# Kernel optimization log

Measured on AMD Instinct MI355X. Metric: run time of the kernel, lower is better.

The kernel has to match this reference:

```python
import jax, jax.numpy as jnp
import numpy as np

N_POS, D_MODEL, D_SAE, TOP_K = 2, 1024, 32768, 32


def setup_inputs() -> dict:
    key = jax.random.key(0)
    k_x, k_we, k_wd = jax.random.split(key, 3)
    x = jax.random.normal(k_x, (4096, N_POS, D_MODEL), dtype=jnp.float32)
    W_enc = jax.random.normal(k_we, (N_POS, D_MODEL, D_SAE), dtype=jnp.float32) * (1.0 / D_MODEL ** 0.5)
    W_dec = jax.random.normal(k_wd, (D_SAE, N_POS, D_MODEL), dtype=jnp.float32) * (1.0 / D_SAE ** 0.5)
    b_enc = jnp.zeros((D_SAE,), dtype=jnp.float32)
    b_dec = jnp.zeros((N_POS, D_MODEL), dtype=jnp.float32)
    return {"x": x, "W_enc": W_enc, "W_dec": W_dec, "b_enc": b_enc, "b_dec": b_dec}


def reference(x, W_enc, W_dec, b_enc, b_dec):
    # Encode: per-position einsum then shared bias -> (batch, d_sae)
    pre_act = jnp.einsum('btd,tds->bs', x, W_enc) + b_enc
    top_vals, top_idx = jax.lax.top_k(pre_act, TOP_K)  # (b, k)
    batch = pre_act.shape[0]
    rows = jnp.arange(batch)[:, None]  # (b, 1) broadcast against (b, k)
    z = jnp.zeros_like(pre_act).at[rows, top_idx].set(jax.nn.relu(top_vals))
    # Decode: dense contraction over d_sae -> (batch, n_positions, d_model)
    x_hat = jnp.einsum('bs,std->btd', z, W_dec) + b_dec
    return x_hat
```

## Files before the change

### kernel.cpp

```cpp
#include <hip/hip_runtime.h>
#include <cstdint>
#include <cstddef>

typedef unsigned short u16;
typedef unsigned long long u64;
typedef __attribute__((ext_vector_type(8))) short short8;
typedef __attribute__((ext_vector_type(4))) float f32x4;

constexpr int K_DIM = 2048;
constexpr int S_DIM = 32768;
constexpr int TOPK  = 32;
constexpr int CAP   = 256;
#define EPS      0.06f
#define THR_EMIT 3.7f
#define HIST_LO  3.5f

__device__ __forceinline__ u16 f2bf(float f) {
    unsigned u = __float_as_uint(f);
    return (u16)((u + 0x7FFFu + ((u >> 16) & 1u)) >> 16);
}
__device__ __forceinline__ unsigned key_map(float f) {
    unsigned u = __float_as_uint(f);
    return (u & 0x80000000u) ? ~u : (u | 0x80000000u);
}
__device__ __forceinline__ float key_unmap(unsigned k) {
    unsigned u = (k & 0x80000000u) ? (k ^ 0x80000000u) : ~k;
    return __uint_as_float(u);
}

__global__ __launch_bounds__(256) void init_kernel(int* __restrict__ flag, int M)
{
    int i = blockIdx.x * 256 + threadIdx.x;
    if (i < M) flag[i] = 0;
}

__global__ __launch_bounds__(256) void conv_x_kernel(
    const float* __restrict__ x, u16* __restrict__ hi, int n4)
{
    int i = blockIdx.x * 256 + threadIdx.x;
    if (i >= n4) return;
    float4 v = ((const float4*)x)[i];
    ushort4 h;
    h.x = f2bf(v.x); h.y = f2bf(v.y); h.z = f2bf(v.z); h.w = f2bf(v.w);
    ((ushort4*)hi)[i] = h;
}

__global__ __launch_bounds__(256) void conv_wt_kernel(
    const float* __restrict__ W, float* __restrict__ WT, u16* __restrict__ Wh)
{
    __shared__ float tile[64][65];
    const int t  = threadIdx.x;
    const int s0 = blockIdx.x * 64;
    const int k0 = blockIdx.y * 64;
#pragma unroll
    for (int i = 0; i < 4; ++i) {
        int kl = (t >> 4) + i * 16;
        int sc = (t & 15) * 4;
        float4 v = *(const float4*)&W[(size_t)(k0 + kl) * S_DIM + s0 + sc];
        tile[kl][sc] = v.x; tile[kl][sc + 1] = v.y;
        tile[kl][sc + 2] = v.z; tile[kl][sc + 3] = v.w;
    }
    __syncthreads();
    const int klc = (t & 7) * 8;
#pragma unroll
    for (int i = 0; i < 2; ++i) {
        int sl = (t >> 3) + i * 32;
        float f[8];
        short8 h8;
#pragma unroll
        for (int j = 0; j < 8; ++j) {
            f[j] = tile[klc + j][sl];
            h8[j] = (short)f2bf(f[j]);
        }
        size_t o = (size_t)(s0 + sl) * K_DIM + k0 + klc;
        *(float4*)&WT[o]     = make_float4(f[0], f[1], f[2], f[3]);
        *(float4*)&WT[o + 4] = make_float4(f[4], f[5], f[6], f[7]);
        *(short8*)&Wh[o] = h8;
    }
}

__device__ __forceinline__ void gl16(const u16* g, u16* s) {
    __builtin_amdgcn_global_load_lds(
        (const __attribute__((address_space(1))) unsigned int*)g,
        (__attribute__((address_space(3))) unsigned int*)s,
        16, 0, 0);
}

#define LGKM0  do { asm volatile("s_waitcnt lgkmcnt(0)" ::: "memory"); \
                    __builtin_amdgcn_sched_barrier(0); } while (0)
#define VMW(n) asm volatile("s_waitcnt vmcnt(" #n ")" ::: "memory")
#define BAR    do { __builtin_amdgcn_s_barrier(); \
                    __builtin_amdgcn_sched_barrier(0); } while (0)

__global__ __launch_bounds__(512, 2) void gemm_mfma_kernel(
    const u16* __restrict__ A, const u16* __restrict__ B,
    const float* __restrict__ bias, float* __restrict__ C)
{
    __shared__ alignas(16) u16 sA[2][256 * 64];
    __shared__ alignas(16) u16 sB[2][256 * 64];

    const int t = threadIdx.x;
    const int lane = t & 63;
    const int w = t >> 6;
    const int wm = w >> 2, wn = w & 3;

    const int nwg = gridDim.x;
    const int q = nwg >> 3;
    const int bid = blockIdx.x;
    const int wg = (bid & 7) * q + (bid >> 3);
    const int bm = wg >> 7;
    const int bn = wg & 127;

    const u16* Ab = A + (size_t)bm * 256 * K_DIM;
    const u16* Bb = B + (size_t)bn * 256 * K_DIM;

    const int w2  = w * 2;
    const int lr3 = lane >> 3;
    const int csw = ((lane & 7) ^ lr3) * 8;

    const int rl = lane & 15, kq = lane >> 4;
    const int swz = rl & 7;
    const int ac0 = (kq ^ swz) * 8;
    const int ac1 = ((4 + kq) ^ swz) * 8;
    const int arow = (wm * 16 + rl) * 64;
    const int brow = (wn * 16 + rl) * 64;

    f32x4 acc[8][4];
#pragma unroll
    for (int m = 0; m < 8; ++m)
#pragma unroll
        for (int n = 0; n < 4; ++n) acc[m][n] = (f32x4){0.f, 0.f, 0.f, 0.f};

    auto stA = [&](int half, int j, int kt, int buf) {
        const u16* src = Ab + (size_t)(half * 128 + (w2 + j) * 8 + lr3) * K_DIM
                            + kt * 64 + csw;
        gl16(src, &sA[buf][half * 8192 + (w2 + j) * 512]);
    };
    auto stB = [&](int half, int j, int kt, int buf) {
        const u16* src = Bb + (size_t)(half * 128 + (w2 + j) * 8 + lr3) * K_DIM
                            + kt * 64 + csw;
        gl16(src, &sB[buf][half * 8192 + (w2 + j) * 512]);
    };

    stB(0, 0, 0, 0); stB(0, 1, 0, 0);
    stA(0, 0, 0, 0); stA(0, 1, 0, 0);
    stB(1, 0, 0, 0); stB(1, 1, 0, 0);
    stA(1, 0, 0, 0); stA(1, 1, 0, 0);
    stB(0, 0, 1, 1); stB(0, 1, 1, 1);
    stA(0, 0, 1, 1); stA(0, 1, 1, 1);
    stB(1, 0, 1, 1); stB(1, 1, 1, 1);
    VMW(6);
    BAR;

    short8 af[4][2], bf[4][2];

#pragma unroll 1
    for (int it = 0; it < 16; ++it) {
        const bool lastIt = (it == 15);
#pragma unroll
        for (int h = 0; h < 2; ++h) {
            const int b  = h;
            const int tA = 2 * it + 1 + h;
            const int tB = 2 * it + 2 + h;

#pragma unroll
            for (int m = 0; m < 4; ++m) {
                af[m][0] = *(const short8*)&sA[b][arow + m * 2048 + ac0];
                af[m][1] = *(const short8*)&sA[b][arow + m * 2048 + ac1];
            }
#pragma unroll
            for (int n = 0; n < 2; ++n) {
                bf[n][0] = *(const short8*)&sB[b][brow + n * 4096 + ac0];
                bf[n][1] = *(const short8*)&sB[b][brow + n * 4096 + ac1];
            }
            if (tA < 32) { stA(1, 0, tA, b ^ 1); stA(1, 1, tA, b ^ 1); }
            __builtin_amdgcn_s_barrier();
            LGKM0;
            __builtin_amdgcn_s_setprio(1);
#pragma unroll
            for (int m = 0; m < 4; ++m)
#pragma unroll
                for (int n = 0; n < 2; ++n)
#pragma unroll
                    for (int kk = 0; kk < 2; ++kk)
                        acc[m][n] = __builtin_amdgcn_mfma_f32_16x16x32_bf16(
                            af[m][kk], bf[n][kk], acc[m][n], 0, 0, 0);
            __builtin_amdgcn_s_setprio(0);
            BAR;

#pragma unroll
            for (int n = 2; n < 4; ++n) {
                bf[n][0] = *(const short8*)&sB[b][brow + n * 4096 + ac0];
                bf[n][1] = *(const short8*)&sB[b][brow + n * 4096 + ac1];
            }
            if (tB < 32) { stB(0, 0, tB, b); stB(0, 1, tB, b); }
            __builtin_amdgcn_s_barrier();
            LGKM0;
            __builtin_amdgcn_s_setprio(1);
#pragma unroll
            for (int m = 0; m < 4; ++m)
#pragma unroll
                for (int n = 2; n < 4; ++n)
#pragma unroll
                    for (int kk = 0; kk < 2; ++kk)
                        acc[m][n] = __builtin_amdgcn_mfma_f32_16x16x32_bf16(
                            af[m][kk], bf[n][kk], acc[m][n], 0, 0, 0);
            __builtin_amdgcn_s_setprio(0);
            BAR;

#pragma unroll
            for (int m = 0; m < 4; ++m) {
                af[m][0] = *(const short8*)&sA[b][arow + (m + 4) * 2048 + ac0];
                af[m][1] = *(const short8*)&sA[b][arow + (m + 4) * 2048 + ac1];
            }
            if (tB < 32) { stA(0, 0, tB, b); stA(0, 1, tB, b); }
            __builtin_amdgcn_s_barrier();
            LGKM0;
            __builtin_amdgcn_s_setprio(1);
#pragma unroll
            for (int m = 0; m < 4; ++m)
#pragma unroll
                for (int n = 2; n < 4; ++n)
#pragma unroll
                    for (int kk = 0; kk < 2; ++kk)
                        acc[m + 4][n] = __builtin_amdgcn_mfma_f32_16x16x32_bf16(
                            af[m][kk], bf[n][kk], acc[m + 4][n], 0, 0, 0);
            __builtin_amdgcn_s_setprio(0);
            BAR;

            if (tB < 32) { stB(1, 0, tB, b); stB(1, 1, tB, b); }
            __builtin_amdgcn_s_barrier();
            __builtin_amdgcn_s_setprio(1);
#pragma unroll
            for (int m = 0; m < 4; ++m)
#pragma unroll
                for (int n = 0; n < 2; ++n)
#pragma unroll
                    for (int kk = 0; kk < 2; ++kk)
                        acc[m + 4][n] = __builtin_amdgcn_mfma_f32_16x16x32_bf16(
                            af[m][kk], bf[n][kk], acc[m + 4][n], 0, 0, 0);
            __builtin_amdgcn_s_setprio(0);
            if (lastIt && h == 0) { VMW(0); } else { VMW(6); }
            BAR;
        }
    }

    const int colB = bn * 256 + wn * 16 + rl;
    const size_t rowB = (size_t)bm * 256 + wm * 16 + kq * 4;
    float bv[4];
#pragma unroll
    for (int n = 0; n < 4; ++n) bv[n] = bias[colB + n * 64];
#pragma unroll
    for (int m = 0; m < 8; ++m)
#pragma unroll
        for (int n = 0; n < 4; ++n)
#pragma unroll
            for (int rr = 0; rr < 4; ++rr)
                C[(rowB + m * 32 + rr) * S_DIM + colB + n * 64] =
                    acc[m][n][rr] + bv[n];
}

__global__ __launch_bounds__(256) void screen_kernel(
    const float* __restrict__ pre, u64* __restrict__ emit,
    int* __restrict__ ccnt, float* __restrict__ thrv,
    int* __restrict__ flag, int row0)
{
    __shared__ unsigned hist[64];
    __shared__ int cnt;

    const int t = threadIdx.x;
    const int row = blockIdx.x;
    const int grow = row0 + row;
    const float* prow = pre + (size_t)row * S_DIM;

    if (t < 64) hist[t] = 0;
    if (t == 0) cnt = 0;
    __syncthreads();

    u64* erow = emit + (size_t)grow * CAP;
    for (int i = t * 4; i < S_DIM; i += 1024) {
        float4 v = *(const float4*)(prow + i);
        float vv[4] = {v.x, v.y, v.z, v.w};
#pragma unroll
        for (int j = 0; j < 4; ++j) {
            if (vv[j] >= HIST_LO) {
                int b = (int)((vv[j] - HIST_LO) * 25.0f);
                if (b > 63) b = 63;
                atomicAdd(&hist[b], 1u);
                if (vv[j] >= THR_EMIT) {
                    int p = atomicAdd(&cnt, 1);
                    if (p < CAP)
                        erow[p] = ((u64)key_map(vv[j]) << 32) | (unsigned)(i + j);
                }
            }
        }
    }
    __syncthreads();

    if (t == 0) {
        unsigned acc = 0;
        int b = -1;
        for (int j = 63; j >= 0; --j) {
            acc += hist[j];
            if (acc >= (unsigned)TOPK) { b = j; break; }
        }
        float thr = HIST_LO + 0.04f * b - 2.0f * EPS - 1e-4f;
        if (b < 0 || cnt > CAP || thr < THR_EMIT) {
            flag[grow] = 1;
            thr = THR_EMIT;
        }
        thrv[grow] = thr;
        ccnt[grow] = (cnt < CAP) ? cnt : CAP;
    }
}

__global__ __launch_bounds__(256) void rescore_kernel(
    const float* __restrict__ x, const float* __restrict__ WT,
    const float* __restrict__ benc, const u64* __restrict__ emit,
    const int* __restrict__ ccnt, const float* __restrict__ thrv,
    float* __restrict__ resc, int row0)
{
    const int row = row0 + blockIdx.x;
    const int t = threadIdx.x;
    const int w = t >> 6, l = t & 63;
    const int cnt = ccnt[row];
    const float thr = thrv[row];

    __shared__ float xs[K_DIM];
    const float* xr = x + (size_t)row * K_DIM;
    for (int i = t * 4; i < K_DIM; i += 1024)
        *(float4*)&xs[i] = *(const float4*)&xr[i];
    __syncthreads();

    for (int c = w; c < cnt; c += 4) {
        const u64 pk = emit[(size_t)row * CAP + c];
        const float approx = key_unmap((unsigned)(pk >> 32));
        if (approx < thr) {
            if (l == 0) resc[(size_t)row * CAP + c] = -3e38f;
            continue;
        }
        const int s = (int)(pk & 0xFFFFFFFFu);
        const float* wc = WT + (size_t)s * K_DIM;
        float acc = 0.f;
#pragma unroll
        for (int j = 0; j < 32; ++j)
            acc = fmaf(xs[l + 64 * j], wc[l + 64 * j], acc);
#pragma unroll
        for (int d = 1; d < 64; d <<= 1) acc += __shfl_xor(acc, d);
        if (l == 0) resc[(size_t)row * CAP + c] = acc + benc[s];
    }
}

__global__ __launch_bounds__(64) void select_kernel(
    const float* __restrict__ resc, const u64* __restrict__ emit,
    const int* __restrict__ ccnt, const float* __restrict__ thrv,
    float* __restrict__ tv, int* __restrict__ ti, int* __restrict__ flag,
    int row0)
{
    const int row = row0 + blockIdx.x;
    const int l = threadIdx.x;
    const int cnt = ccnt[row];

    float v[4] = {0.f, 0.f, 0.f, 0.f};
    int   s[4] = {-1, -1, -1, -1};
    u64   p[4] = {0, 0, 0, 0};
#pragma unroll
    for (int j = 0; j < 4; ++j) {
        int c = l + j * 64;
        if (c < cnt) {
            s[j] = (int)(emit[(size_t)row * CAP + c] & 0xFFFFFFFFu);
            v[j] = resc[(size_t)row * CAP + c];
            p[j] = ((u64)key_map(v[j]) << 32) | (unsigned)(~s[j]);
        }
    }

    float* tvr = tv + (size_t)row * TOPK;
    int*   tir = ti + (size_t)row * TOPK;
    float v32f = -3e38f;
#pragma unroll 1
    for (int r = 0; r < TOPK; ++r) {
        u64 m = p[0];
        if (p[1] > m) m = p[1];
        if (p[2] > m) m = p[2];
        if (p[3] > m) m = p[3];
#pragma unroll
        for (int d = 1; d < 64; d <<= 1) {
            u64 o = __shfl_xor(m, d);
            if (o > m) m = o;
        }
        if (r == TOPK - 1) v32f = key_unmap((unsigned)(m >> 32));
        if (p[0] == m)      { tvr[r] = v[0]; tir[r] = s[0] < 0 ? 0 : s[0]; p[0] = 0; }
        else if (p[1] == m) { tvr[r] = v[1]; tir[r] = s[1] < 0 ? 0 : s[1]; p[1] = 0; }
        else if (p[2] == m) { tvr[r] = v[2]; tir[r] = s[2] < 0 ? 0 : s[2]; p[2] = 0; }
        else if (p[3] == m) { tvr[r] = v[3]; tir[r] = s[3] < 0 ? 0 : s[3]; p[3] = 0; }
    }
    if (l == 0) {
        if (v32f < thrv[row] + EPS) flag[row] = 1;
    }
}

__global__ __launch_bounds__(256) void fb_screen_kernel(
    const float* __restrict__ pre, u64* __restrict__ emit,
    int* __restrict__ ccnt, const int* __restrict__ flag, int row0)
{
    const int grow = row0 + blockIdx.x;
    if (!flag[grow]) return;

    __shared__ unsigned hist[2048];
    __shared__ unsigned partial[256];
    __shared__ unsigned sh_tk;
    __shared__ int cnt;

    const int t = threadIdx.x;
    const float* prow = pre + (size_t)blockIdx.x * S_DIM;

    for (int i = t; i < 2048; i += 256) hist[i] = 0;
    if (t == 0) cnt = 0;
    __syncthreads();

    for (int i = t * 4; i < S_DIM; i += 1024) {
        float4 v = *(const float4*)(prow + i);
        unsigned k0 = key_map(v.x), k1 = key_map(v.y),
                 k2 = key_map(v.z), k3 = key_map(v.w);
        if (k0 >= 0xC0000000u) atomicAdd(&hist[(k0 >> 19) - 6144], 1u);
        if (k1 >= 0xC0000000u) atomicAdd(&hist[(k1 >> 19) - 6144], 1u);
        if (k2 >= 0xC0000000u) atomicAdd(&hist[(k2 >> 19) - 6144], 1u);
        if (k3 >= 0xC0000000u) atomicAdd(&hist[(k3 >> 19) - 6144], 1u);
    }
    __syncthreads();

    unsigned ps = 0;
#pragma unroll
    for (int j = 0; j < 8; ++j) ps += hist[t * 8 + j];
    partial[t] = ps;
    __syncthreads();

    if (t == 0) {
        unsigned acc = 0;
        int seg = -1;
        for (int s = 255; s >= 0; --s) {
            if (acc + partial[s] >= (unsigned)TOPK) { seg = s; break; }
            acc += partial[s];
        }
        int bucket = 6144;
        if (seg >= 0) {
            for (int b = seg * 8 + 7; b >= seg * 8; --b) {
                acc += hist[b];
                if (acc >= (unsigned)TOPK) { bucket = 6144 + b; break; }
            }
        }
        float lo = key_unmap(((unsigned)bucket) << 19) - 2.0f * EPS;
        sh_tk = key_map(lo);
    }
    __syncthreads();

    const unsigned TK = sh_tk;
    u64* erow = emit + (size_t)grow * CAP;
    for (int i = t * 4; i < S_DIM; i += 1024) {
        float4 v = *(const float4*)(prow + i);
        unsigned k[4] = {key_map(v.x), key_map(v.y), key_map(v.z), key_map(v.w)};
#pragma unroll
        for (int j = 0; j < 4; ++j)
            if (k[j] >= TK) {
                int p = atomicAdd(&cnt, 1);
                if (p < CAP) erow[p] = ((u64)k[j] << 32) | (unsigned)(i + j);
            }
    }
    __syncthreads();
    if (t == 0) ccnt[grow] = (cnt < CAP) ? cnt : CAP;
}

__global__ __launch_bounds__(256) void fb_rescore_kernel(
    const float* __restrict__ x, const float* __restrict__ WT,
    const float* __restrict__ benc, const u64* __restrict__ emit,
    const int* __restrict__ ccnt, float* __restrict__ resc,
    const int* __restrict__ flag, int row0)
{
    const int row = row0 + blockIdx.x;
    if (!flag[row]) return;
    const int t = threadIdx.x;
    const int w = t >> 6, l = t & 63;
    const int cnt = ccnt[row];

    __shared__ float xs[K_DIM];
    const float* xr = x + (size_t)row * K_DIM;
    for (int i = t * 4; i < K_DIM; i += 1024)
        *(float4*)&xs[i] = *(const float4*)&xr[i];
    __syncthreads();

    for (int c = w; c < cnt; c += 4) {
        const int s = (int)(emit[(size_t)row * CAP + c] & 0xFFFFFFFFu);
        const float* wc = WT + (size_t)s * K_DIM;
        float acc = 0.f;
#pragma unroll
        for (int j = 0; j < 32; ++j)
            acc = fmaf(xs[l + 64 * j], wc[l + 64 * j], acc);
#pragma unroll
        for (int d = 1; d < 64; d <<= 1) acc += __shfl_xor(acc, d);
        if (l == 0) resc[(size_t)row * CAP + c] = acc + benc[s];
    }
}

__global__ __launch_bounds__(64) void fb_select_kernel(
    const float* __restrict__ resc, const u64* __restrict__ emit,
    const int* __restrict__ ccnt, float* __restrict__ tv,
    int* __restrict__ ti, const int* __restrict__ flag, int row0)
{
    const int row = row0 + blockIdx.x;
    if (!flag[row]) return;
    const int l = threadIdx.x;
    const int cnt = ccnt[row];

    float v[4] = {0.f, 0.f, 0.f, 0.f};
    int   s[4] = {-1, -1, -1, -1};
    u64   p[4] = {0, 0, 0, 0};
#pragma unroll
    for (int j = 0; j < 4; ++j) {
        int c = l + j * 64;
        if (c < cnt) {
            s[j] = (int)(emit[(size_t)row * CAP + c] & 0xFFFFFFFFu);
            v[j] = resc[(size_t)row * CAP + c];
            p[j] = ((u64)key_map(v[j]) << 32) | (unsigned)(~s[j]);
        }
    }

    float* tvr = tv + (size_t)row * TOPK;
    int*   tir = ti + (size_t)row * TOPK;
#pragma unroll 1
    for (int r = 0; r < TOPK; ++r) {
        u64 m = p[0];
        if (p[1] > m) m = p[1];
        if (p[2] > m) m = p[2];
        if (p[3] > m) m = p[3];
#pragma unroll
        for (int d = 1; d < 64; d <<= 1) {
            u64 o = __shfl_xor(m, d);
            if (o > m) m = o;
        }
        if (p[0] == m)      { tvr[r] = v[0]; tir[r] = s[0] < 0 ? 0 : s[0]; p[0] = 0; }
        else if (p[1] == m) { tvr[r] = v[1]; tir[r] = s[1] < 0 ? 0 : s[1]; p[1] = 0; }
        else if (p[2] == m) { tvr[r] = v[2]; tir[r] = s[2] < 0 ? 0 : s[2]; p[2] = 0; }
        else if (p[3] == m) { tvr[r] = v[3]; tir[r] = s[3] < 0 ? 0 : s[3]; p[3] = 0; }
    }
}

__global__ __launch_bounds__(256) void decode_kernel(
    const float* __restrict__ tval, const int* __restrict__ tidx,
    const float* __restrict__ Wd, const float* __restrict__ bdec,
    float* __restrict__ out, int row0)
{
    const int row = row0 + blockIdx.x;
    const int t = threadIdx.x;
    __shared__ float sv[TOPK];
    __shared__ int   si[TOPK];
    if (t < TOPK) {
        sv[t] = fmaxf(tval[(size_t)row * TOPK + t], 0.f);
        si[t] = tidx[(size_t)row * TOPK + t];
    }
    __syncthreads();

    const int c0 = t * 4;
    float4 acc0 = *(const float4*)(bdec + c0);
    float4 acc1 = *(const float4*)(bdec + 1024 + c0);
#pragma unroll 4
    for (int i = 0; i < TOPK; ++i) {
        const float z = sv[i];
        if (z > 0.f) {
            const float* wr = Wd + (size_t)si[i] * K_DIM;
            float4 w0 = *(const float4*)(wr + c0);
            float4 w1 = *(const float4*)(wr + 1024 + c0);
            acc0.x = fmaf(z, w0.x, acc0.x); acc0.y = fmaf(z, w0.y, acc0.y);
            acc0.z = fmaf(z, w0.z, acc0.z); acc0.w = fmaf(z, w0.w, acc0.w);
            acc1.x = fmaf(z, w1.x, acc1.x); acc1.y = fmaf(z, w1.y, acc1.y);
            acc1.z = fmaf(z, w1.z, acc1.z); acc1.w = fmaf(z, w1.w, acc1.w);
        }
    }
    float* op = out + (size_t)row * K_DIM;
    *(float4*)(op + c0) = acc0;
    *(float4*)(op + 1024 + c0) = acc1;
}

extern "C" void kernel_launch(void* const* d_in, const int* in_sizes, int n_in,
                              void* d_out, int out_size, void* d_ws, size_t ws_size,
                              hipStream_t stream)
{
    const float* x     = (const float*)d_in[0];
    const float* W_enc = (const float*)d_in[1];
    const float* W_dec = (const float*)d_in[2];
    const float* b_enc = (const float*)d_in[3];
    const float* b_dec = (const float*)d_in[4];
    float* out = (float*)d_out;

    const int M = in_sizes[0] / K_DIM;

    char* wsb = (char*)d_ws;
    size_t o = 0;
    float*    tv   = (float*)(wsb + o);    o += (size_t)M * TOPK * 4;
    int*      ti   = (int*)(wsb + o);      o += (size_t)M * TOPK * 4;
    u64*      emit = (u64*)(wsb + o);      o += (size_t)M * CAP * 8;
    int*      ccnt = (int*)(wsb + o);      o += (size_t)M * 4;
    float*    thrv = (float*)(wsb + o);    o += (size_t)M * 4;
    int*      flag = (int*)(wsb + o);      o += (size_t)M * 4;
    float*    resc = (float*)(wsb + o);    o += (size_t)M * CAP * 4;
    u16*      Xh   = (u16*)(wsb + o);      o += (size_t)M * K_DIM * 2;
    u16*      Wh   = (u16*)(wsb + o);      o += (size_t)S_DIM * K_DIM * 2;
    float*    WT   = (float*)(wsb + o);    o += (size_t)S_DIM * K_DIM * 4;
    float*    pre  = (float*)(wsb + o);

    size_t cap = (ws_size > o) ? (ws_size - o) : 0;
    long cap_rows = (long)(cap / ((size_t)S_DIM * 4));
    int chunk = (int)((cap_rows / 256) * 256);
    if (chunk <= 0) chunk = 256;
    if (chunk > M) chunk = M;

    init_kernel<<<(M + 255) / 256, 256, 0, stream>>>(flag, M);
    const int n4 = M * K_DIM / 4;
    conv_x_kernel<<<(n4 + 255) / 256, 256, 0, stream>>>(x, Xh, n4);
    conv_wt_kernel<<<dim3(S_DIM / 64, K_DIM / 64), 256, 0, stream>>>(W_enc, WT, Wh);

    for (int r0 = 0; r0 < M; r0 += chunk) {
        const int rows = (M - r0 < chunk) ? (M - r0) : chunk;
        const int nbm = rows / 256;
        gemm_mfma_kernel<<<nbm * 128, 512, 0, stream>>>(
            Xh + (size_t)r0 * K_DIM, Wh, b_enc, pre);
        screen_kernel<<<rows, 256, 0, stream>>>(pre, emit, ccnt, thrv, flag, r0);
        rescore_kernel<<<rows, 256, 0, stream>>>(x, WT, b_enc, emit, ccnt, thrv, resc, r0);
        select_kernel<<<rows, 64, 0, stream>>>(resc, emit, ccnt, thrv, tv, ti, flag, r0);
        fb_screen_kernel<<<rows, 256, 0, stream>>>(pre, emit, ccnt, flag, r0);
        fb_rescore_kernel<<<rows, 256, 0, stream>>>(x, WT, b_enc, emit, ccnt, resc, flag, r0);
        fb_select_kernel<<<rows, 64, 0, stream>>>(resc, emit, ccnt, tv, ti, flag, r0);
        decode_kernel<<<rows, 256, 0, stream>>>(tv, ti, W_dec, b_dec, out, r0);
    }
}
```

Before: 1.234 ms.

## Store encoder pre-activations as bf16 via LDS-staged coalesced epilogue

The GEMM epilogue now rounds pre-activations to bf16 and stages them through shared memory, then writes each output row with coalesced 16-byte stores instead of scattered fp32 writes. The screen and fallback screen kernels read bf16 values eight at a time, which halves the bytes of the large pre-activation matrix that is written and then read twice. Because bf16 screening is less precise, the rescore margin EPS is widened. The risks are more borderline candidates reaching the fp32 rescore and possible missed top-k entries if the bf16 rounding exceeds the margin.

New measurement: 1.086 ms. -11.9%, faster.

```diff
diff --git a/kernel.cpp b/kernel.cpp
--- a/kernel.cpp
+++ b/kernel.cpp
@@ -11,13 +11,16 @@
 constexpr int S_DIM = 32768;
 constexpr int TOPK  = 32;
 constexpr int CAP   = 256;
-#define EPS      0.06f
+#define EPS      0.07f
 #define THR_EMIT 3.7f
 #define HIST_LO  3.5f
 
 __device__ __forceinline__ u16 f2bf(float f) {
     unsigned u = __float_as_uint(f);
     return (u16)((u + 0x7FFFu + ((u >> 16) & 1u)) >> 16);
+}
+__device__ __forceinline__ float bf2f(u16 h) {
+    return __uint_as_float(((unsigned)h) << 16);
 }
 __device__ __forceinline__ unsigned key_map(float f) {
     unsigned u = __float_as_uint(f);
@@ -94,10 +97,11 @@
 
 __global__ __launch_bounds__(512, 2) void gemm_mfma_kernel(
     const u16* __restrict__ A, const u16* __restrict__ B,
-    const float* __restrict__ bias, float* __restrict__ C)
-{
-    __shared__ alignas(16) u16 sA[2][256 * 64];
-    __shared__ alignas(16) u16 sB[2][256 * 64];
+    const float* __restrict__ bias, u16* __restrict__ Cb)
+{
+    __shared__ alignas(16) u16 sMem[65536];
+    u16* sA0 = sMem;
+    u16* sB0 = sMem + 32768;
 
     const int t = threadIdx.x;
     const int lane = t & 63;
@@ -134,12 +138,12 @@
     auto stA = [&](int half, int j, int kt, int buf) {
         const u16* src = Ab + (size_t)(half * 128 + (w2 + j) * 8 + lr3) * K_DIM
                             + kt * 64 + csw;
-        gl16(src, &sA[buf][half * 8192 + (w2 + j) * 512]);
+        gl16(src, sA0 + buf * 16384 + half * 8192 + (w2 + j) * 512);
     };
     auto stB = [&](int half, int j, int kt, int buf) {
         const u16* src = Bb + (size_t)(half * 128 + (w2 + j) * 8 + lr3) * K_DIM
                             + kt * 64 + csw;
-        gl16(src, &sB[buf][half * 8192 + (w2 + j) * 512]);
+        gl16(src, sB0 + buf * 16384 + half * 8192 + (w2 + j) * 512);
     };
 
     stB(0, 0, 0, 0); stB(0, 1, 0, 0);
@@ -165,13 +169,13 @@
 
 #pragma unroll
             for (int m = 0; m < 4; ++m) {
-                af[m][0] = *(const short8*)&sA[b][arow + m * 2048 + ac0];
-                af[m][1] = *(const short8*)&sA[b][arow + m * 2048 + ac1];
+                af[m][0] = *(const short8*)&sA0[b * 16384 + arow + m * 2048 + ac0];
+                af[m][1] = *(const short8*)&sA0[b * 16384 + arow + m * 2048 + ac1];
             }
 #pragma unroll
             for (int n = 0; n < 2; ++n) {
-                bf[n][0] = *(const short8*)&sB[b][brow + n * 4096 + ac0];
-                bf[n][1] = *(const short8*)&sB[b][brow + n * 4096 + ac1];
+                bf[n][0] = *(const short8*)&sB0[b * 16384 + brow + n * 4096 + ac0];
+                bf[n][1] = *(const short8*)&sB0[b * 16384 + brow + n * 4096 + ac1];
             }
             if (tA < 32) { stA(1, 0, tA, b ^ 1); stA(1, 1, tA, b ^ 1); }
             __builtin_amdgcn_s_barrier();
@@ -190,8 +194,8 @@
 
 #pragma unroll
             for (int n = 2; n < 4; ++n) {
-                bf[n][0] = *(const short8*)&sB[b][brow + n * 4096 + ac0];
-                bf[n][1] = *(const short8*)&sB[b][brow + n * 4096 + ac1];
+                bf[n][0] = *(const short8*)&sB0[b * 16384 + brow + n * 4096 + ac0];
+                bf[n][1] = *(const short8*)&sB0[b * 16384 + brow + n * 4096 + ac1];
             }
             if (tB < 32) { stB(0, 0, tB, b); stB(0, 1, tB, b); }
             __builtin_amdgcn_s_barrier();
@@ -210,8 +214,8 @@
 
 #pragma unroll
             for (int m = 0; m < 4; ++m) {
-                af[m][0] = *(const short8*)&sA[b][arow + (m + 4) * 2048 + ac0];
-                af[m][1] = *(const short8*)&sA[b][arow + (m + 4) * 2048 + ac1];
+                af[m][0] = *(const short8*)&sA0[b * 16384 + arow + (m + 4) * 2048 + ac0];
+                af[m][1] = *(const short8*)&sA0[b * 16384 + arow + (m + 4) * 2048 + ac1];
             }
             if (tB < 32) { stA(0, 0, tB, b); stA(0, 1, tB, b); }
             __builtin_amdgcn_s_barrier();
@@ -245,23 +249,36 @@
         }
     }
 
-    const int colB = bn * 256 + wn * 16 + rl;
-    const size_t rowB = (size_t)bm * 256 + wm * 16 + kq * 4;
-    float bv[4];
-#pragma unroll
-    for (int n = 0; n < 4; ++n) bv[n] = bias[colB + n * 64];
-#pragma unroll
-    for (int m = 0; m < 8; ++m)
-#pragma unroll
-        for (int n = 0; n < 4; ++n)
-#pragma unroll
-            for (int rr = 0; rr < 4; ++rr)
-                C[(rowB + m * 32 + rr) * S_DIM + colB + n * 64] =
-                    acc[m][n][rr] + bv[n];
+    {
+        const int colL = wn * 16 + rl;
+        const int rowL = wm * 16 + kq * 4;
+        float bv[4];
+#pragma unroll
+        for (int n = 0; n < 4; ++n) bv[n] = bias[bn * 256 + colL + n * 64];
+#pragma unroll
+        for (int m = 0; m < 8; ++m)
+#pragma unroll
+            for (int n = 0; n < 4; ++n)
+#pragma unroll
+                for (int rr = 0; rr < 4; ++rr)
+                    sMem[(rowL + m * 32 + rr) * 256 + colL + n * 64] =
+                        f2bf(acc[m][n][rr] + bv[n]);
+        __syncthreads();
+
+        const int rr2 = t >> 5;
+        const int c16 = t & 31;
+        const size_t growB = (size_t)bm * 256;
+#pragma unroll
+        for (int r = 0; r < 16; ++r) {
+            const int lrow = r * 16 + rr2;
+            short8 v = *(const short8*)&sMem[lrow * 256 + c16 * 8];
+            *(short8*)&Cb[(growB + lrow) * S_DIM + bn * 256 + c16 * 8] = v;
+        }
+    }
 }
 
 __global__ __launch_bounds__(256) void screen_kernel(
-    const float* __restrict__ pre, u64* __restrict__ emit,
+    const u16* __restrict__ pre, u64* __restrict__ emit,
     int* __restrict__ ccnt, float* __restrict__ thrv,
     int* __restrict__ flag, int row0)
 {
@@ -271,26 +288,26 @@
     const int t = threadIdx.x;
     const int row = blockIdx.x;
     const int grow = row0 + row;
-    const float* prow = pre + (size_t)row * S_DIM;
+    const u16* prow = pre + (size_t)row * S_DIM;
 
     if (t < 64) hist[t] = 0;
     if (t == 0) cnt = 0;
     __syncthreads();
 
     u64* erow = emit + (size_t)grow * CAP;
-    for (int i = t * 4; i < S_DIM; i += 1024) {
-        float4 v = *(const float4*)(prow + i);
-        float vv[4] = {v.x, v.y, v.z, v.w};
-#pragma unroll
-        for (int j = 0; j < 4; ++j) {
-            if (vv[j] >= HIST_LO) {
-                int b = (int)((vv[j] - HIST_LO) * 25.0f);
+    for (int i = t * 8; i < S_DIM; i += 2048) {
+        short8 v8 = *(const short8*)&prow[i];
+#pragma unroll
+        for (int j = 0; j < 8; ++j) {
+            float v = bf2f((u16)v8[j]);
+            if (v >= HIST_LO) {
+                int b = (int)((v - HIST_LO) * 25.0f);
                 if (b > 63) b = 63;
                 atomicAdd(&hist[b], 1u);
-                if (vv[j] >= THR_EMIT) {
+                if (v >= THR_EMIT) {
                     int p = atomicAdd(&cnt, 1);
                     if (p < CAP)
-                        erow[p] = ((u64)key_map(vv[j]) << 32) | (unsigned)(i + j);
+                        erow[p] = ((u64)key_map(v) << 32) | (unsigned)(i + j);
                 }
             }
         }
@@ -400,7 +417,7 @@
 }
 
 __global__ __launch_bounds__(256) void fb_screen_kernel(
-    const float* __restrict__ pre, u64* __restrict__ emit,
+    const u16* __restrict__ pre, u64* __restrict__ emit,
     int* __restrict__ ccnt, const int* __restrict__ flag, int row0)
 {
     const int grow = row0 + blockIdx.x;
@@ -412,20 +429,19 @@
     __shared__ int cnt;
 
     const int t = threadIdx.x;
-    const float* prow = pre + (size_t)blockIdx.x * S_DIM;
+    const u16* prow = pre + (size_t)blockIdx.x * S_DIM;
 
     for (int i = t; i < 2048; i += 256) hist[i] = 0;
     if (t == 0) cnt = 0;
     __syncthreads();
 
-    for (int i = t * 4; i < S_DIM; i += 1024) {
-        float4 v = *(const float4*)(prow + i);
-        unsigned k0 = key_map(v.x), k1 = key_map(v.y),
-                 k2 = key_map(v.z), k3 = key_map(v.w);
-        if (k0 >= 0xC0000000u) atomicAdd(&hist[(k0 >> 19) - 6144], 1u);
-        if (k1 >= 0xC0000000u) atomicAdd(&hist[(k1 >> 19) - 6144], 1u);
-        if (k2 >= 0xC0000000u) atomicAdd(&hist[(k2 >> 19) - 6144], 1u);
-        if (k3 >= 0xC0000000u) atomicAdd(&hist[(k3 >> 19) - 6144], 1u);
+    for (int i = t * 8; i < S_DIM; i += 2048) {
+        short8 v8 = *(const short8*)&prow[i];
+#pragma unroll
+        for (int j = 0; j < 8; ++j) {
+            unsigned k = key_map(bf2f((u16)v8[j]));
+            if (k >= 0xC0000000u) atomicAdd(&hist[(k >> 19) - 6144], 1u);
+        }
     }
     __syncthreads();
 
@@ -456,15 +472,16 @@
 
     const unsigned TK = sh_tk;
     u64* erow = emit + (size_t)grow * CAP;
-    for (int i = t * 4; i < S_DIM; i += 1024) {
-        float4 v = *(const float4*)(prow + i);
-        unsigned k[4] = {key_map(v.x), key_map(v.y), key_map(v.z), key_map(v.w)};
-#pragma unroll
-        for (int j = 0; j < 4; ++j)
-            if (k[j] >= TK) {
+    for (int i = t * 8; i < S_DIM; i += 2048) {
+        short8 v8 = *(const short8*)&prow[i];
+#pragma unroll
+        for (int j = 0; j < 8; ++j) {
+            unsigned k = key_map(bf2f((u16)v8[j]));
+            if (k >= TK) {
                 int p = atomicAdd(&cnt, 1);
-                if (p < CAP) erow[p] = ((u64)k[j] << 32) | (unsigned)(i + j);
+                if (p < CAP) erow[p] = ((u64)k << 32) | (unsigned)(i + j);
             }
+        }
     }
     __syncthreads();
     if (t == 0) ccnt[grow] = (cnt < CAP) ? cnt : CAP;
@@ -605,10 +622,10 @@
     u16*      Xh   = (u16*)(wsb + o);      o += (size_t)M * K_DIM * 2;
     u16*      Wh   = (u16*)(wsb + o);      o += (size_t)S_DIM * K_DIM * 2;
     float*    WT   = (float*)(wsb + o);    o += (size_t)S_DIM * K_DIM * 4;
-    float*    pre  = (float*)(wsb + o);
+    u16*      pre  = (u16*)(wsb + o);
 
     size_t cap = (ws_size > o) ? (ws_size - o) : 0;
-    long cap_rows = (long)(cap / ((size_t)S_DIM * 4));
+    long cap_rows = (long)(cap / ((size_t)S_DIM * 2));
     int chunk = (int)((cap_rows / 256) * 256);
     if (chunk <= 0) chunk = 256;
     if (chunk > M) chunk = M;
```
